# Performance work log

Measured on AMD Instinct MI355X. Metric: run time of the kernel, lower is better.

The kernel has to match this reference:

```python
import jax, jax.numpy as jnp
import numpy as np

D_MODEL = 1024
N_HEADS = 16
D_HEAD = 64
B, S = 2, 2048


def setup_inputs() -> dict:
    key = jax.random.key(0)
    ks = jax.random.split(key, 16)
    HDH = N_HEADS * D_HEAD
    s = 0.02
    return {
        "h": jax.random.normal(ks[0], (B, S, D_MODEL), dtype=jnp.float32),
        "att_mask": jax.random.randint(ks[1], (B, S), 0, 2) > 0,
        "Wq": jax.random.normal(ks[2], (D_MODEL, HDH), dtype=jnp.float32) * s,
        "bq": jnp.zeros((HDH,), dtype=jnp.float32),
        "Wkv": jax.random.normal(ks[3], (D_MODEL, 2 * HDH), dtype=jnp.float32) * s,
        "bkv": jnp.zeros((2 * HDH,), dtype=jnp.float32),
        "Wo": jax.random.normal(ks[4], (HDH, D_MODEL), dtype=jnp.float32) * s,
        "bo": jnp.zeros((D_MODEL,), dtype=jnp.float32),
        "W1": jax.random.normal(ks[5], (D_MODEL, D_MODEL), dtype=jnp.float32) * s,
        "b1": jnp.zeros((D_MODEL,), dtype=jnp.float32),
        "W2": jax.random.normal(ks[6], (D_MODEL, D_MODEL), dtype=jnp.float32) * s,
        "b2": jnp.zeros((D_MODEL,), dtype=jnp.float32),
        "ln_g": jnp.ones((D_MODEL,), dtype=jnp.float32),
        "ln_b": jnp.zeros((D_MODEL,), dtype=jnp.float32),
    }


def _layer_norm(x, g, b, eps=1e-6):
    mu = jnp.mean(x, axis=-1, keepdims=True)
    var = jnp.mean(jnp.square(x - mu), axis=-1, keepdims=True)
    return (x - mu) * jax.lax.rsqrt(var + eps) * g + b


def reference(h, att_mask, Wq, bq, Wkv, bkv, Wo, bo, W1, b1, W2, b2, ln_g, ln_b):
    bz, ln, _ = h.shape
    scale = 1.0 / (D_HEAD ** 0.5)
    q = (h @ Wq + bq).reshape(bz, ln, N_HEADS, D_HEAD)
    kv = h @ Wkv + bkv
    k, v = jnp.split(kv, 2, axis=-1)
    k = k.reshape(bz, ln, N_HEADS, D_HEAD)
    v = v.reshape(bz, ln, N_HEADS, D_HEAD)
    # scores: [b, heads, len_q, len_k]
    scores = jnp.einsum('bqhd,bkhd->bhqk', q, k) * scale
    scores = jnp.where(att_mask[:, None, None, :], -1e9, scores)
    probs = jax.nn.softmax(scores, axis=-1)
    att = jnp.einsum('bhqk,bkhd->bqhd', probs, v).reshape(bz, ln, N_HEADS * D_HEAD)
    att_out = att @ Wo + bo
    # glu_type == 1
    g = jax.nn.sigmoid(h @ W1 + b1) * (h @ W2 + b2)
    return _layer_norm(h + att_out + g, ln_g, ln_b)
```

## Files before the change

### kernel.cpp

```cpp
#include <hip/hip_runtime.h>
#include <hip/hip_bf16.h>


typedef short bf16x8 __attribute__((ext_vector_type(8)));
typedef float f32x4  __attribute__((ext_vector_type(4)));
typedef float f32x16 __attribute__((ext_vector_type(16)));
typedef unsigned int u32x4 __attribute__((ext_vector_type(4)));

typedef const __attribute__((address_space(1))) void* gas_cvp;
typedef __attribute__((address_space(3))) void* las_vp;

__device__ __forceinline__ void gload_lds16(const void* g, void* l) {
  __builtin_amdgcn_global_load_lds((gas_cvp)g, (las_vp)l, 16, 0, 0);
}

__device__ __forceinline__ short f2bf(float f) {
  __hip_bfloat16 h = __float2bfloat16(f);
  return *reinterpret_cast<short*>(&h);
}
__device__ __forceinline__ float bf2f(short s) {
  unsigned u = ((unsigned)(unsigned short)s) << 16;
  return __builtin_bit_cast(float, u);
}

#if __has_builtin(__builtin_amdgcn_exp2f)
#define EXP2(x) __builtin_amdgcn_exp2f(x)
#else
#define EXP2(x) exp2f(x)
#endif

constexpr int BATCH = 2;
constexpr int SEQ   = 2048;
constexpr int NH    = 16;
constexpr int MROWS = BATCH * SEQ;
constexpr int NSPLIT = 4;
constexpr int KSPL   = SEQ / NSPLIT;
constexpr int RH     = MROWS * NH;


__global__ __launch_bounds__(256) void cvt_bf16(const float* __restrict__ src,
                                                short* __restrict__ dst, int n4) {
  int i = blockIdx.x * 256 + threadIdx.x;
  if (i >= n4) return;
  float4 v = reinterpret_cast<const float4*>(src)[i];
  short4 o;
  o.x = f2bf(v.x); o.y = f2bf(v.y); o.z = f2bf(v.z); o.w = f2bf(v.w);
  reinterpret_cast<short4*>(dst)[i] = o;
}

struct WtA {
  const float* s[6];
  short* d[6];
  int st[6];
  int mul[6];
  int add[6];
};
__global__ __launch_bounds__(256) void wtrans6(WtA a) {
  __shared__ float tile[32][33];
  const float* __restrict__ src = a.s[blockIdx.z];
  short* __restrict__ dst = a.d[blockIdx.z];
  const int stride = a.st[blockIdx.z];
  const int mul = a.mul[blockIdx.z], add = a.add[blockIdx.z];
  const int tx = threadIdx.x & 31, ty = threadIdx.x >> 5;
  const int n0 = blockIdx.x * 32, k0 = blockIdx.y * 32;
  #pragma unroll
  for (int i = 0; i < 32; i += 8)
    tile[ty + i][tx] = src[(size_t)(k0 + ty + i) * stride + n0 + tx];
  __syncthreads();
  #pragma unroll
  for (int i = 0; i < 32; i += 8)
    dst[(size_t)((n0 + ty + i) * mul + add) * 1024 + k0 + tx] = f2bf(tile[tx][ty + i]);
}

__global__ __launch_bounds__(256) void vtrans(const short* __restrict__ qkv,
                                              short* __restrict__ vt) {
  __shared__ short tile[32][33];
  const int tx = threadIdx.x & 31, ty = threadIdx.x >> 5;
  const int s0 = blockIdx.x * 32, d0 = blockIdx.y * 32, b = blockIdx.z;
  #pragma unroll
  for (int i = 0; i < 32; i += 8)
    tile[ty + i][tx] = qkv[(size_t)(b * SEQ + s0 + ty + i) * 3072 + 2048 + d0 + tx];
  __syncthreads();
  #pragma unroll
  for (int i = 0; i < 32; i += 8)
    vt[(size_t)(b * 1024 + d0 + ty + i) * SEQ + s0 + tx] = tile[tx][ty + i];
}

__global__ void pack_bias(const float* __restrict__ bq, const float* __restrict__ bkv,
                          const float* __restrict__ b1, const float* __restrict__ b2,
                          float* __restrict__ bqkv, float* __restrict__ b12i) {
  int i = blockIdx.x * 256 + threadIdx.x;
  if (i < 1024) bqkv[i] = bq[i];
  else if (i < 3072) bqkv[i] = bkv[i - 1024];
  else if (i < 4096) {
    const int j = i - 3072;
    b12i[2 * j] = b1[j];
    b12i[2 * j + 1] = b2[j];
  }
}

__device__ __forceinline__ bool mask_at(const void* mp, int idx, int flag) {
  if (flag == 1) return ((const int*)mp)[idx] != 0;
  if (flag == 2) return ((const float*)mp)[idx] != 0.f;
  return ((const unsigned char*)mp)[idx] != 0;
}

__global__ __launch_bounds__(256) void premask(const void* __restrict__ msk,
                                               float* __restrict__ mbL) {
  __shared__ int si, sf;
  const unsigned* m = (const unsigned*)msk;
  if (threadIdx.x == 0) { si = 1; sf = 1; }
  __syncthreads();
  bool oki = true, okf = true;
  for (int i = threadIdx.x; i < 1024; i += 256) {
    unsigned v = m[i];
    oki = oki && (v <= 1u);
    okf = okf && (v == 0u || v == 0x3F800000u);
  }
  if (!oki) si = 0;
  if (!okf) sf = 0;
  __syncthreads();
  const int flag = si ? 1 : (sf ? 2 : 0);
  int i = blockIdx.x * 256 + threadIdx.x;
  if (i < MROWS) mbL[i] = mask_at(msk, i, flag) ? -1.442695e9f : -8.0f;
}

template <int EPI>
__global__ __launch_bounds__(256) void gemm_kernel(const short* __restrict__ A,
                                                   const short* __restrict__ BT,
                                                   const float* __restrict__ bias,
                                                   short* __restrict__ outp, int N) {
  __shared__ short Alds[4096];
  __shared__ short Blds[4096];
  const int tid = threadIdx.x;
  const int w = tid >> 6, lane = tid & 63, g = lane >> 4, lr = lane & 15;
  const int wr = w >> 1, wc = w & 1;
  const int bm = blockIdx.y, bn = blockIdx.x;

  f32x4 acc[4][4] = {};

  const int srow = tid >> 2;
  const int scol = (tid & 3) * 8;
  const short* Ab = A  + (size_t)(bm * 128 + srow) * 1024 + scol;
  const short* Bb = BT + (size_t)(bn * 128 + srow) * 1024 + scol;

  for (int kt = 0; kt < 32; ++kt) {
    const int kb = kt * 32;
    __syncthreads();
    gload_lds16(Ab + kb,             &Alds[tid * 8]);
    gload_lds16(Ab + 64 * 1024 + kb, &Alds[2048 + tid * 8]);
    gload_lds16(Bb + kb,             &Blds[tid * 8]);
    gload_lds16(Bb + 64 * 1024 + kb, &Blds[2048 + tid * 8]);
    asm volatile("s_waitcnt vmcnt(0)" ::: "memory");
    __syncthreads();

    bf16x8 af[4], bfr[4];
    #pragma unroll
    for (int m = 0; m < 4; ++m)
      af[m] = *reinterpret_cast<const bf16x8*>(&Alds[(wr * 64 + m * 16 + lr) * 32 + g * 8]);
    #pragma unroll
    for (int n = 0; n < 4; ++n)
      bfr[n] = *reinterpret_cast<const bf16x8*>(&Blds[(wc * 64 + n * 16 + lr) * 32 + g * 8]);
    #pragma unroll
    for (int m = 0; m < 4; ++m)
      #pragma unroll
      for (int n = 0; n < 4; ++n)
        acc[m][n] = __builtin_amdgcn_mfma_f32_16x16x32_bf16(af[m], bfr[n], acc[m][n], 0, 0, 0);
  }

  #pragma unroll
  for (int m = 0; m < 4; ++m) {
    const int row = bm * 128 + wr * 64 + m * 16 + g * 4;
    #pragma unroll
    for (int n = 0; n < 4; ++n) {
      const int col = bn * 128 + wc * 64 + n * 16 + lr;
      const float bv = bias[col];
      #pragma unroll
      for (int r = 0; r < 4; ++r) {
        const float v = acc[m][n][r] + bv;
        if constexpr (EPI == 0) {
          outp[(size_t)(row + r) * N + col] = f2bf(v);
        } else {
          const float vp = __shfl_xor(v, 1);
          if (!(lr & 1))
            outp[(size_t)(row + r) * (N / 2) + (col >> 1)] =
                f2bf(vp / (1.f + __expf(-v)));
        }
      }
    }
  }
}

constexpr int KB = 64;
constexpr int KSLOT = 8 * 66;
constexpr int VSLOT = 8 * 66;

__global__ __launch_bounds__(256) void attn_kernel(const short* __restrict__ qkv,
                                                   const short* __restrict__ vt,
                                                   const float* __restrict__ mbL,
                                                   short* __restrict__ opart,
                                                   float* __restrict__ spart) {
  __shared__ short Kl[2][KSLOT * 8];
  __shared__ short Vl[2][VSLOT * 8];
  __shared__ float mb[KSPL];

  const int tid = threadIdx.x;
  const int w = tid >> 6, lane = tid & 63, ql = lane & 31, hi = lane >> 5;
  const int sp = blockIdx.x & (NSPLIT - 1), qb = blockIdx.x / NSPLIT;
  const int h = blockIdx.y, b = blockIdx.z;
  const int qrow = qb * 128 + w * 32 + ql;
  const int kofs = sp * KSPL;

  bf16x8 qf[4];
  {
    const short* qp = qkv + (size_t)(b * SEQ + qrow) * 3072 + h * 64;
    #pragma unroll
    for (int c = 0; c < 4; ++c)
      qf[c] = *reinterpret_cast<const bf16x8*>(qp + c * 16 + hi * 8);
  }

  const short* gkbase = qkv + (size_t)(b * SEQ + kofs) * 3072 + 1024 + h * 64
                        + (size_t)(tid >> 3) * 3072 + (tid & 7) * 8;
  const short* gvbase = vt + ((size_t)(b * 1024 + h * 64) + (tid >> 3)) * SEQ + kofs
                        + (tid & 7) * 8;
  short* kwr = &Kl[0][((tid & 7) * 66 + (tid >> 3)) * 8];
  short* vwr = &Vl[0][((tid & 7) * 66 + (tid >> 3)) * 8];

  u32x4 kreg0, kreg1, vreg0, vreg1;
  auto loadTile = [&](int kt) {
    const short* gk = gkbase + (size_t)kt * KB * 3072;
    kreg0 = *reinterpret_cast<const u32x4*>(gk);
    kreg1 = *reinterpret_cast<const u32x4*>(gk + 32 * 3072);
    const short* gv = gvbase + kt * KB;
    vreg0 = *reinterpret_cast<const u32x4*>(gv);
    vreg1 = *reinterpret_cast<const u32x4*>(gv + 32 * SEQ);
  };
  auto writeTile = [&](int buf) {
    short* kd = kwr + buf * KSLOT * 8;
    *reinterpret_cast<u32x4*>(kd)          = kreg0;
    *reinterpret_cast<u32x4*>(kd + 32 * 8) = kreg1;
    short* vd = vwr + buf * VSLOT * 8;
    *reinterpret_cast<u32x4*>(vd)          = vreg0;
    *reinterpret_cast<u32x4*>(vd + 32 * 8) = vreg1;
  };

  float s_run = 0.f;
  f32x16 oacc0 = {}, oacc1 = {};

  if (tid < 128) gload_lds16(mbL + b * SEQ + kofs + tid * 4, &mb[tid * 4]);
  loadTile(0);
  writeTile(0);
  __syncthreads();

  const short* krd = &Kl[0][(hi * 66 + ql) * 8];
  const short* vrd = &Vl[0][(hi * 66 + ql) * 8];

  constexpr int NT = KSPL / KB;
  for (int kt = 0; kt < NT; ++kt) {
    const int cur = kt & 1;
    if (kt + 1 < NT) loadTile(kt + 1);
    const short* Kb = krd + cur * KSLOT * 8;
    const short* Vb = vrd + cur * VSLOT * 8;

    #pragma unroll
    for (int t2 = 0; t2 < 2; ++t2) {
      f32x16 sc = {};
      __builtin_amdgcn_s_setprio(1);
      #pragma unroll
      for (int c = 0; c < 4; ++c) {
        bf16x8 kf = *reinterpret_cast<const bf16x8*>(Kb + (c * 132 + t2 * 32) * 8);
        sc = __builtin_amdgcn_mfma_f32_32x32x16_bf16(kf, qf[c], sc, 0, 0, 0);
      }
      __builtin_amdgcn_s_setprio(0);
      float p[16];
      #pragma unroll
      for (int u = 0; u < 4; ++u) {
        float4 m4 = *reinterpret_cast<const float4*>(&mb[kt * KB + t2 * 32 + u * 8 + hi * 4]);
        p[4 * u + 0] = EXP2(fmaf(sc[4 * u + 0], 0.18033688f, m4.x));
        p[4 * u + 1] = EXP2(fmaf(sc[4 * u + 1], 0.18033688f, m4.y));
        p[4 * u + 2] = EXP2(fmaf(sc[4 * u + 2], 0.18033688f, m4.z));
        p[4 * u + 3] = EXP2(fmaf(sc[4 * u + 3], 0.18033688f, m4.w));
      }
      {
        float a0 = (p[0] + p[1]) + (p[2] + p[3]);
        float a1 = (p[4] + p[5]) + (p[6] + p[7]);
        float a2 = (p[8] + p[9]) + (p[10] + p[11]);
        float a3 = (p[12] + p[13]) + (p[14] + p[15]);
        s_run += (a0 + a1) + (a2 + a3);
      }
      unsigned P[8];
      #pragma unroll
      for (int j = 0; j < 8; ++j)
        asm("v_cvt_pk_bf16_f32 %0, %1, %2" : "=v"(P[j]) : "v"(p[2 * j]), "v"(p[2 * j + 1]));
      asm("v_permlane32_swap_b32 %0, %1" : "+v"(P[0]), "+v"(P[2]));
      asm("v_permlane32_swap_b32 %0, %1" : "+v"(P[1]), "+v"(P[3]));
      asm("v_permlane32_swap_b32 %0, %1" : "+v"(P[4]), "+v"(P[6]));
      asm("v_permlane32_swap_b32 %0, %1" : "+v"(P[5]), "+v"(P[7]));
      u32x4 c0 = { P[0], P[1], P[2], P[3] };
      u32x4 c1 = { P[4], P[5], P[6], P[7] };
      bf16x8 pf[2] = { __builtin_bit_cast(bf16x8, c0), __builtin_bit_cast(bf16x8, c1) };

      __builtin_amdgcn_s_setprio(1);
      #pragma unroll
      for (int ch = 0; ch < 2; ++ch) {
        const int gb = (t2 * 4 + ch * 2) * 66;
        bf16x8 v0 = *reinterpret_cast<const bf16x8*>(Vb + gb * 8);
        bf16x8 v1 = *reinterpret_cast<const bf16x8*>(Vb + (gb + 32) * 8);
        oacc0 = __builtin_amdgcn_mfma_f32_32x32x16_bf16(v0, pf[ch], oacc0, 0, 0, 0);
        oacc1 = __builtin_amdgcn_mfma_f32_32x32x16_bf16(v1, pf[ch], oacc1, 0, 0, 0);
      }
      __builtin_amdgcn_s_setprio(0);
    }

    if (kt + 1 < NT) {
      writeTile(cur ^ 1);
      __syncthreads();
    }
  }

  const float sT = s_run + __shfl_xor(s_run, 32);
  const size_t obase = (size_t)sp * RH * 64 + (size_t)(b * SEQ + qrow) * 1024 + h * 64;
  #pragma unroll
  for (int dt = 0; dt < 2; ++dt) {
    #pragma unroll
    for (int u = 0; u < 4; ++u) {
      short4 st;
      const f32x16& oa = dt ? oacc1 : oacc0;
      st.x = f2bf(oa[4 * u + 0]);
      st.y = f2bf(oa[4 * u + 1]);
      st.z = f2bf(oa[4 * u + 2]);
      st.w = f2bf(oa[4 * u + 3]);
      *reinterpret_cast<short4*>(&opart[obase + dt * 32 + u * 8 + hi * 4]) = st;
    }
  }
  if (hi == 0)
    spart[sp * RH + (b * SEQ + qrow) * NH + h] = sT;
}

__global__ __launch_bounds__(256) void attn_merge(const short* __restrict__ opart,
                                                  const float* __restrict__ spart,
                                                  short* __restrict__ att) {
  const int idx = blockIdx.x * 256 + threadIdx.x;
  const int rh = idx >> 3;
  const size_t base = (size_t)rh * 64 + (idx & 7) * 8;
  float acc[8] = {};
  float ss = 0.f;
  #pragma unroll
  for (int s = 0; s < NSPLIT; ++s) {
    bf16x8 o = *reinterpret_cast<const bf16x8*>(&opart[(size_t)s * RH * 64 + base]);
    #pragma unroll
    for (int j = 0; j < 8; ++j) acc[j] += bf2f(o[j]);
    ss += spart[s * RH + rh];
  }
  const float inv = 1.f / ss;
  bf16x8 r;
  #pragma unroll
  for (int j = 0; j < 8; ++j) r[j] = f2bf(acc[j] * inv);
  *reinterpret_cast<bf16x8*>(&att[base]) = r;
}

__global__ __launch_bounds__(256) void ln_kernel(const float* __restrict__ h,
                                                 const short* __restrict__ ao,
                                                 const short* __restrict__ gl,
                                                 const float* __restrict__ gamma,
                                                 const float* __restrict__ beta,
                                                 float* __restrict__ out) {
  const int row = blockIdx.x;
  const size_t base = (size_t)row * 1024;
  const int t = threadIdx.x;
  __shared__ float red[4];
  float x[4];
  #pragma unroll
  for (int j = 0; j < 4; ++j) {
    const int c = t + j * 256;
    x[j] = h[base + c] + bf2f(ao[base + c]) + bf2f(gl[base + c]);
  }
  float s = x[0] + x[1] + x[2] + x[3];
  #pragma unroll
  for (int d = 1; d < 64; d <<= 1) s += __shfl_xor(s, d);
  if ((t & 63) == 0) red[t >> 6] = s;
  __syncthreads();
  const float mu = (red[0] + red[1] + red[2] + red[3]) * (1.f / 1024.f);
  __syncthreads();
  float vs = 0.f;
  #pragma unroll
  for (int j = 0; j < 4; ++j) { const float dx = x[j] - mu; vs += dx * dx; }
  #pragma unroll
  for (int d = 1; d < 64; d <<= 1) vs += __shfl_xor(vs, d);
  if ((t & 63) == 0) red[t >> 6] = vs;
  __syncthreads();
  const float var = (red[0] + red[1] + red[2] + red[3]) * (1.f / 1024.f);
  const float rs = rsqrtf(var + 1e-6f);
  #pragma unroll
  for (int j = 0; j < 4; ++j) {
    const int c = t + j * 256;
    out[base + c] = (x[j] - mu) * rs * gamma[c] + beta[c];
  }
}


extern "C" void kernel_launch(void* const* d_in, const int* in_sizes, int n_in,
                              void* d_out, int out_size, void* d_ws, size_t ws_size,
                              hipStream_t stream) {
  const float* h   = (const float*)d_in[0];
  const void*  msk = d_in[1];
  const float* Wq  = (const float*)d_in[2];
  const float* bq  = (const float*)d_in[3];
  const float* Wkv = (const float*)d_in[4];
  const float* bkv = (const float*)d_in[5];
  const float* Wo  = (const float*)d_in[6];
  const float* bo  = (const float*)d_in[7];
  const float* W1  = (const float*)d_in[8];
  const float* b1  = (const float*)d_in[9];
  const float* W2  = (const float*)d_in[10];
  const float* b2  = (const float*)d_in[11];
  const float* lng = (const float*)d_in[12];
  const float* lnb = (const float*)d_in[13];
  float* out = (float*)d_out;

  char* ws = (char*)d_ws;
  size_t off = 0;
  auto alloc = [&](size_t bytes) {
    char* p = ws + off;
    off += (bytes + 255) & ~(size_t)255;
    return p;
  };
  short* X     = (short*)alloc((size_t)MROWS * 1024 * 2);
  short* WqkvT = (short*)alloc((size_t)3072 * 1024 * 2);
  short* WoT   = (short*)alloc((size_t)1024 * 1024 * 2);
  short* W12T  = (short*)alloc((size_t)2048 * 1024 * 2);
  float* bqkv  = (float*)alloc(3072 * 4);
  float* b12i  = (float*)alloc(2048 * 4);
  float* MBL   = (float*)alloc((size_t)MROWS * 4);
  short* QKV   = (short*)alloc((size_t)MROWS * 3072 * 2);
  short* VT    = (short*)alloc((size_t)BATCH * 1024 * SEQ * 2);
  short* ATT   = (short*)alloc((size_t)MROWS * 1024 * 2);
  short* X1    = (short*)alloc((size_t)MROWS * 1024 * 2);
  short* AO    = (short*)alloc((size_t)MROWS * 1024 * 2);
  short* OP    = (short*)alloc((size_t)NSPLIT * RH * 64 * 2);
  float* SP    = (float*)alloc((size_t)NSPLIT * RH * 4);
  if (off > ws_size) return;

  cvt_bf16<<<4096, 256, 0, stream>>>(h, X, MROWS * 1024 / 4);
  WtA wa;
  wa.s[0] = Wq;          wa.d[0] = WqkvT;                wa.st[0] = 1024;  wa.mul[0] = 1; wa.add[0] = 0;
  wa.s[1] = Wkv;         wa.d[1] = WqkvT + 1024 * 1024;  wa.st[1] = 2048;  wa.mul[1] = 1; wa.add[1] = 0;
  wa.s[2] = Wkv + 1024;  wa.d[2] = WqkvT + 2048 * 1024;  wa.st[2] = 2048;  wa.mul[2] = 1; wa.add[2] = 0;
  wa.s[3] = Wo;          wa.d[3] = WoT;                  wa.st[3] = 1024;  wa.mul[3] = 1; wa.add[3] = 0;
  wa.s[4] = W1;          wa.d[4] = W12T;                 wa.st[4] = 1024;  wa.mul[4] = 2; wa.add[4] = 0;
  wa.s[5] = W2;          wa.d[5] = W12T;                 wa.st[5] = 1024;  wa.mul[5] = 2; wa.add[5] = 1;
  wtrans6<<<dim3(32, 32, 6), 256, 0, stream>>>(wa);
  pack_bias<<<16, 256, 0, stream>>>(bq, bkv, b1, b2, bqkv, b12i);
  premask<<<16, 256, 0, stream>>>(msk, MBL);

  gemm_kernel<0><<<dim3(24, 32), 256, 0, stream>>>(X, WqkvT, bqkv, QKV, 3072);
  vtrans<<<dim3(64, 32, 2), 256, 0, stream>>>(QKV, VT);
  attn_kernel<<<dim3(16 * NSPLIT, 16, 2), 256, 0, stream>>>(QKV, VT, MBL, OP, SP);
  attn_merge<<<RH * 8 / 256, 256, 0, stream>>>(OP, SP, ATT);
  gemm_kernel<1><<<dim3(16, 32), 256, 0, stream>>>(X, W12T, b12i, X1, 2048);
  gemm_kernel<0><<<dim3(8, 32), 256, 0, stream>>>(ATT, WoT, bo, AO, 1024);
  ln_kernel<<<MROWS, 256, 0, stream>>>(h, AO, X1, lng, lnb, out);
}
```

Baseline: 179.0 us.

## Fuse QKV and GLU GEMMs into one launch, narrow Wo tiles, halve attention splits

Concatenates the QKV and W1/W2 weights and biases so a single GEMM launch of 40x32 blocks produces both the QKV projection and the gated GLU output, choosing the epilogue per block column. The Wo projection gets a BN=64 tile variant, doubling its block count to improve occupancy. Attention key splits drop from 4 to 2, halving partial outputs and merge work but lowering parallelism in the attention kernel. The mask preload now uses all 256 threads to fill the larger per-split mask buffer.

```diff
diff --git a/kernel.cpp b/kernel.cpp
--- a/kernel.cpp
+++ b/kernel.cpp
@@ -33,7 +33,7 @@
 constexpr int SEQ   = 2048;
 constexpr int NH    = 16;
 constexpr int MROWS = BATCH * SEQ;
-constexpr int NSPLIT = 4;
+constexpr int NSPLIT = 2;
 constexpr int KSPL   = SEQ / NSPLIT;
 constexpr int RH     = MROWS * NH;
 
@@ -88,14 +88,14 @@
 
 __global__ void pack_bias(const float* __restrict__ bq, const float* __restrict__ bkv,
                           const float* __restrict__ b1, const float* __restrict__ b2,
-                          float* __restrict__ bqkv, float* __restrict__ b12i) {
+                          float* __restrict__ ball) {
   int i = blockIdx.x * 256 + threadIdx.x;
-  if (i < 1024) bqkv[i] = bq[i];
-  else if (i < 3072) bqkv[i] = bkv[i - 1024];
+  if (i < 1024) ball[i] = bq[i];
+  else if (i < 3072) ball[i] = bkv[i - 1024];
   else if (i < 4096) {
     const int j = i - 3072;
-    b12i[2 * j] = b1[j];
-    b12i[2 * j + 1] = b2[j];
+    ball[3072 + 2 * j] = b1[j];
+    ball[3072 + 2 * j + 1] = b2[j];
   }
 }
 
@@ -125,11 +125,70 @@
   if (i < MROWS) mbL[i] = mask_at(msk, i, flag) ? -1.442695e9f : -8.0f;
 }
 
-template <int EPI>
-__global__ __launch_bounds__(256) void gemm_kernel(const short* __restrict__ A,
+template <int BN>
+__global__ __launch_bounds__(256) void gemm_bf16(const short* __restrict__ A,
+                                                 const short* __restrict__ BT,
+                                                 const float* __restrict__ bias,
+                                                 short* __restrict__ outp, int N) {
+  constexpr int NF = BN / 32;
+  __shared__ short Alds[4096];
+  __shared__ short Blds[BN * 32];
+  const int tid = threadIdx.x;
+  const int w = tid >> 6, lane = tid & 63, g = lane >> 4, lr = lane & 15;
+  const int wr = w >> 1, wc = w & 1;
+  const int bm = blockIdx.y, bn = blockIdx.x;
+
+  f32x4 acc[4][NF] = {};
+
+  const int srow = tid >> 2;
+  const int scol = (tid & 3) * 8;
+  const short* Ab = A  + (size_t)(bm * 128 + srow) * 1024 + scol;
+  const short* Bb = BT + (size_t)(bn * BN + srow) * 1024 + scol;
+
+  for (int kt = 0; kt < 32; ++kt) {
+    const int kb = kt * 32;
+    __syncthreads();
+    gload_lds16(Ab + kb,             &Alds[tid * 8]);
+    gload_lds16(Ab + 64 * 1024 + kb, &Alds[2048 + tid * 8]);
+    gload_lds16(Bb + kb,             &Blds[tid * 8]);
+    if constexpr (BN == 128)
+      gload_lds16(Bb + 64 * 1024 + kb, &Blds[2048 + tid * 8]);
+    asm volatile("s_waitcnt vmcnt(0)" ::: "memory");
+    __syncthreads();
+
+    bf16x8 af[4], bfr[NF];
+    #pragma unroll
+    for (int m = 0; m < 4; ++m)
+      af[m] = *reinterpret_cast<const bf16x8*>(&Alds[(wr * 64 + m * 16 + lr) * 32 + g * 8]);
+    #pragma unroll
+    for (int n = 0; n < NF; ++n)
+      bfr[n] = *reinterpret_cast<const bf16x8*>(&Blds[(wc * (BN / 2) + n * 16 + lr) * 32 + g * 8]);
+    #pragma unroll
+    for (int m = 0; m < 4; ++m)
+      #pragma unroll
+      for (int n = 0; n < NF; ++n)
+        acc[m][n] = __builtin_amdgcn_mfma_f32_16x16x32_bf16(af[m], bfr[n], acc[m][n], 0, 0, 0);
+  }
+
+  #pragma unroll
+  for (int m = 0; m < 4; ++m) {
+    const int row = bm * 128 + wr * 64 + m * 16 + g * 4;
+    #pragma unroll
+    for (int n = 0; n < NF; ++n) {
+      const int col = bn * BN + wc * (BN / 2) + n * 16 + lr;
+      const float bv = bias[col];
+      #pragma unroll
+      for (int r = 0; r < 4; ++r)
+        outp[(size_t)(row + r) * N + col] = f2bf(acc[m][n][r] + bv);
+    }
+  }
+}
+
+__global__ __launch_bounds__(256) void gemm_qkvglu(const short* __restrict__ A,
                                                    const short* __restrict__ BT,
                                                    const float* __restrict__ bias,
-                                                   short* __restrict__ outp, int N) {
+                                                   short* __restrict__ qkv,
+                                                   short* __restrict__ x1) {
   __shared__ short Alds[4096];
   __shared__ short Blds[4096];
   const int tid = threadIdx.x;
@@ -168,6 +227,7 @@
         acc[m][n] = __builtin_amdgcn_mfma_f32_16x16x32_bf16(af[m], bfr[n], acc[m][n], 0, 0, 0);
   }
 
+  const bool isGlu = (bn >= 24);
   #pragma unroll
   for (int m = 0; m < 4; ++m) {
     const int row = bm * 128 + wr * 64 + m * 16 + g * 4;
@@ -178,13 +238,14 @@
       #pragma unroll
       for (int r = 0; r < 4; ++r) {
         const float v = acc[m][n][r] + bv;
-        if constexpr (EPI == 0) {
-          outp[(size_t)(row + r) * N + col] = f2bf(v);
+        if (!isGlu) {
+          qkv[(size_t)(row + r) * 3072 + col] = f2bf(v);
         } else {
           const float vp = __shfl_xor(v, 1);
-          if (!(lr & 1))
-            outp[(size_t)(row + r) * (N / 2) + (col >> 1)] =
-                f2bf(vp / (1.f + __expf(-v)));
+          if (!(lr & 1)) {
+            const int col2 = col - 3072;
+            x1[(size_t)(row + r) * 1024 + (col2 >> 1)] = f2bf(vp / (1.f + __expf(-v)));
+          }
         }
       }
     }
@@ -247,7 +308,7 @@
   float s_run = 0.f;
   f32x16 oacc0 = {}, oacc1 = {};
 
-  if (tid < 128) gload_lds16(mbL + b * SEQ + kofs + tid * 4, &mb[tid * 4]);
+  gload_lds16(mbL + b * SEQ + kofs + tid * 4, &mb[tid * 4]);
   loadTile(0);
   writeTile(0);
   __syncthreads();
@@ -426,11 +487,9 @@
     return p;
   };
   short* X     = (short*)alloc((size_t)MROWS * 1024 * 2);
-  short* WqkvT = (short*)alloc((size_t)3072 * 1024 * 2);
+  short* WALL  = (short*)alloc((size_t)5120 * 1024 * 2);
   short* WoT   = (short*)alloc((size_t)1024 * 1024 * 2);
-  short* W12T  = (short*)alloc((size_t)2048 * 1024 * 2);
-  float* bqkv  = (float*)alloc(3072 * 4);
-  float* b12i  = (float*)alloc(2048 * 4);
+  float* ball  = (float*)alloc(5120 * 4);
   float* MBL   = (float*)alloc((size_t)MROWS * 4);
   short* QKV   = (short*)alloc((size_t)MROWS * 3072 * 2);
   short* VT    = (short*)alloc((size_t)BATCH * 1024 * SEQ * 2);
@@ -443,21 +502,20 @@
 
   cvt_bf16<<<4096, 256, 0, stream>>>(h, X, MROWS * 1024 / 4);
   WtA wa;
-  wa.s[0] = Wq;          wa.d[0] = WqkvT;                wa.st[0] = 1024;  wa.mul[0] = 1; wa.add[0] = 0;
-  wa.s[1] = Wkv;         wa.d[1] = WqkvT + 1024 * 1024;  wa.st[1] = 2048;  wa.mul[1] = 1; wa.add[1] = 0;
-  wa.s[2] = Wkv + 1024;  wa.d[2] = WqkvT + 2048 * 1024;  wa.st[2] = 2048;  wa.mul[2] = 1; wa.add[2] = 0;
-  wa.s[3] = Wo;          wa.d[3] = WoT;                  wa.st[3] = 1024;  wa.mul[3] = 1; wa.add[3] = 0;
-  wa.s[4] = W1;          wa.d[4] = W12T;                 wa.st[4] = 1024;  wa.mul[4] = 2; wa.add[4] = 0;
-  wa.s[5] = W2;          wa.d[5] = W12T;                 wa.st[5] = 1024;  wa.mul[5] = 2; wa.add[5] = 1;
+  wa.s[0] = Wq;          wa.d[0] = WALL;                wa.st[0] = 1024;  wa.mul[0] = 1; wa.add[0] = 0;
+  wa.s[1] = Wkv;         wa.d[1] = WALL + 1024 * 1024;  wa.st[1] = 2048;  wa.mul[1] = 1; wa.add[1] = 0;
+  wa.s[2] = Wkv + 1024;  wa.d[2] = WALL + 2048 * 1024;  wa.st[2] = 2048;  wa.mul[2] = 1; wa.add[2] = 0;
+  wa.s[3] = Wo;          wa.d[3] = WoT;                 wa.st[3] = 1024;  wa.mul[3] = 1; wa.add[3] = 0;
+  wa.s[4] = W1;          wa.d[4] = WALL + 3072 * 1024;  wa.st[4] = 1024;  wa.mul[4] = 2; wa.add[4] = 0;
+  wa.s[5] = W2;          wa.d[5] = WALL + 3072 * 1024;  wa.st[5] = 1024;  wa.mul[5] = 2; wa.add[5] = 1;
   wtrans6<<<dim3(32, 32, 6), 256, 0, stream>>>(wa);
-  pack_bias<<<16, 256, 0, stream>>>(bq, bkv, b1, b2, bqkv, b12i);
+  pack_bias<<<16, 256, 0, stream>>>(bq, bkv, b1, b2, ball);
   premask<<<16, 256, 0, stream>>>(msk, MBL);
 
-  gemm_kernel<0><<<dim3(24, 32), 256, 0, stream>>>(X, WqkvT, bqkv, QKV, 3072);
+  gemm_qkvglu<<<dim3(40, 32), 256, 0, stream>>>(X, WALL, ball, QKV, X1);
   vtrans<<<dim3(64, 32, 2), 256, 0, stream>>>(QKV, VT);
   attn_kernel<<<dim3(16 * NSPLIT, 16, 2), 256, 0, stream>>>(QKV, VT, MBL, OP, SP);
   attn_merge<<<RH * 8 / 256, 256, 0, stream>>>(OP, SP, ATT);
-  gemm_kernel<1><<<dim3(16, 32), 256, 0, stream>>>(X, W12T, b12i, X1, 2048);
-  gemm_kernel<0><<<dim3(8, 32), 256, 0, stream>>>(ATT, WoT, bo, AO, 1024);
+  gemm_bf16<64><<<dim3(16, 32), 256, 0, stream>>>(ATT, WoT, bo, AO, 1024);
   ln_kernel<<<MROWS, 256, 0, stream>>>(h, AO, X1, lng, lnb, out);
 }
```

Result: no change. 175.5 us (-1.9%).
